# Kernel optimization log

Measured on AMD Instinct MI355X. Metric: run time of the kernel, lower is better.

Reference implementation:

```python
import jax, jax.numpy as jnp
import numpy as np

# Paged/ragged causal prefill attention (FlashInfer wrapper.run semantics),
# modeled as equal-length batched causal GQA attention.
B, S = 2, 2048          # batch, seq_len (T = B*S tokens, flattened)
H, HKV, D = 32, 8, 128  # query heads, kv heads, head dim
G = H // HKV            # GQA group size
SCALE = 0.08838834764831845  # 1/sqrt(D)


def setup_inputs() -> dict:
    key = jax.random.key(0)
    kq, kk, kv = jax.random.split(key, 3)
    q = jax.random.normal(kq, (B * S, H * D), dtype=jnp.float32)
    k = jax.random.normal(kk, (B * S, HKV * D), dtype=jnp.float32)
    v = jax.random.normal(kv, (B * S, HKV * D), dtype=jnp.float32)
    return {"q": q, "k": k, "v": v}


def reference(q, k, v):
    # q: [T, H*D] -> [B, S, HKV, G, D]; k, v: [T, HKV*D] -> [B, S, HKV, D]
    qh = q.reshape(B, S, HKV, G, D)
    kh = k.reshape(B, S, HKV, D)
    vh = v.reshape(B, S, HKV, D)
    # GQA attention scores: [B, HKV, G, Sq, Sk]
    scores = jnp.einsum('bqhgd,bkhd->bhgqk', qh, kh) * SCALE
    causal = jnp.tril(jnp.ones((S, S), dtype=bool))  # query attends to keys <= its position
    scores = jnp.where(causal, scores, jnp.finfo(scores.dtype).min)
    probs = jax.nn.softmax(scores, axis=-1)
    out = jnp.einsum('bhgqk,bkhd->bqhgd', probs, vh)
    # back to flattened token layout [T, H*D]
    return out.reshape(B * S, H * D)
```

## Files before the change

### kernel.cpp

```cpp
#include <hip/hip_runtime.h>


#define B_   2
#define S_   2048
#define H_   32
#define HKV_ 8
#define D_   128
#define SCALEF 0.08838834764831845f
#define COEF  (SCALEF * 1.44269504088896340736f)
#define DEFER_THR 8.0f

typedef float          f32x4 __attribute__((ext_vector_type(4)));
typedef __bf16         bf16x2 __attribute__((ext_vector_type(2)));
typedef __bf16         bf16x8 __attribute__((ext_vector_type(8)));
typedef unsigned short u16x8 __attribute__((ext_vector_type(8)));

#define MFMA16(a, b, c) __builtin_amdgcn_mfma_f32_16x16x32_bf16((a), (b), (c), 0, 0, 0)

#if defined(__has_builtin)
#if __has_builtin(__builtin_amdgcn_exp2f)
#define EXP2F(x) __builtin_amdgcn_exp2f(x)
#endif
#endif
#ifndef EXP2F
#define EXP2F(x) exp2f(x)
#endif

static __device__ __forceinline__ unsigned short f2bf(float f) {
  unsigned int u = __builtin_bit_cast(unsigned int, f);
  u = (u + 0x7fffu + ((u >> 16) & 1u)) >> 16;
  return (unsigned short)u;
}

static __device__ __forceinline__ void load_lds16(const void* g, void* l) {
  __builtin_amdgcn_global_load_lds(
      (const __attribute__((address_space(1))) void*)g,
      (__attribute__((address_space(3))) void*)l, 16, 0, 0);
}

template <int CTRL>
static __device__ __forceinline__ float dppf(float v) {
  return __builtin_bit_cast(
      float, __builtin_amdgcn_update_dpp(0, __builtin_bit_cast(int, v), CTRL,
                                         0xF, 0xF, true));
}
static __device__ __forceinline__ float rowmax16(float v) {
  v = fmaxf(v, dppf<0x128>(v));
  v = fmaxf(v, dppf<0x124>(v));
  v = fmaxf(v, dppf<0x122>(v));
  v = fmaxf(v, dppf<0x121>(v));
  return v;
}
static __device__ __forceinline__ float rowsum16(float v) {
  v += dppf<0x128>(v);
  v += dppf<0x124>(v);
  v += dppf<0x122>(v);
  v += dppf<0x121>(v);
  return v;
}

__global__ __launch_bounds__(256) void k_convert_kernel(
    const float* __restrict__ k, unsigned short* __restrict__ kbf) {
  int t = blockIdx.x * 256 + threadIdx.x;
  int o = t * 8;
  int d = o & (D_ - 1);
  int s = (o >> 7) & (S_ - 1);
  int bh = o >> 18;
  int b = bh >> 3, hkv = bh & 7;
  const float* src = k + (size_t)(b * S_ + s) * (HKV_ * D_) + hkv * D_ + d;
  f32x4 x0 = *(const f32x4*)src;
  f32x4 x1 = *(const f32x4*)(src + 4);
  u16x8 w;
  w[0] = f2bf(x0[0]); w[1] = f2bf(x0[1]); w[2] = f2bf(x0[2]); w[3] = f2bf(x0[3]);
  w[4] = f2bf(x1[0]); w[5] = f2bf(x1[1]); w[6] = f2bf(x1[2]); w[7] = f2bf(x1[3]);
  *(u16x8*)(kbf + o) = w;
}

__global__ __launch_bounds__(256) void vt_transpose_kernel(
    const float* __restrict__ v, unsigned short* __restrict__ vt) {
  __shared__ float tile[32][65];
  const int tid = threadIdx.x;
  const int s0 = blockIdx.x * 64;
  const int d0 = blockIdx.y * 32;
  const int bh = blockIdx.z;
  const float* src = v + (size_t)(bh >> 3) * S_ * (HKV_ * D_) + (bh & 7) * D_;
#pragma unroll
  for (int it = 0; it < 8; ++it) {
    int idx = it * 256 + tid;
    int sl = idx >> 5, dl = idx & 31;
    tile[dl][sl] = src[(size_t)(s0 + sl) * (HKV_ * D_) + d0 + dl];
  }
  __syncthreads();
  unsigned int* dst = (unsigned int*)vt;
#pragma unroll
  for (int it = 0; it < 4; ++it) {
    int idx = it * 256 + tid;
    int dl = idx >> 5, sp = idx & 31;
    unsigned int w = (unsigned int)f2bf(tile[dl][2 * sp]) |
                     ((unsigned int)f2bf(tile[dl][2 * sp + 1]) << 16);
    dst[(((size_t)bh * D_ + d0 + dl) * S_ + s0 + 2 * sp) >> 1] = w;
  }
}

#define PSTR 40

__global__ __launch_bounds__(256, 4) void attn_kernel(
    const float* __restrict__ qg, const unsigned short* __restrict__ kbfg,
    const unsigned short* __restrict__ vtg, float* __restrict__ outg) {
  __shared__ unsigned short KL[2][32 * 128];
  __shared__ unsigned short VL[2][128 * 32];
  __shared__ unsigned short PL[4][16 * PSTR];

  const int tid = threadIdx.x;
  const int wave = tid >> 6, lane = tid & 63;
  const int l15 = lane & 15, quad = lane >> 4;

  const int xb = (int)blockIdx.x;
  const int b = (int)(blockIdx.y >> 5), h = (int)(blockIdx.y & 31);
  const int hkv = h >> 2;

  const unsigned short* kbf = kbfg + (size_t)(b * HKV_ + hkv) * S_ * D_;
  const unsigned short* vtb = vtg + (size_t)(b * HKV_ + hkv) * D_ * S_;

  const f32x4 zero4 = {0.f, 0.f, 0.f, 0.f};
  const float NEG_INF = -__builtin_huge_valf();

  auto stage = [&](int kt, int buf) {
#pragma unroll
    for (int j = 0; j < 2; ++j) {
      int si = wave * 128 + j * 64 + lane;
      int kr = si >> 4, pc = si & 15;
      int lc = pc ^ (kr & 15);
      load_lds16(kbf + (size_t)(kt * 32 + kr) * D_ + lc * 8,
                 &KL[buf][(wave * 128 + j * 64) * 8]);
    }
#pragma unroll
    for (int j = 0; j < 2; ++j) {
      int si = wave * 128 + j * 64 + lane;
      int dr = si >> 2, pc = si & 3;
      int lc = pc ^ ((dr >> 1) & 3);
      load_lds16(vtb + (size_t)dr * S_ + kt * 32 + lc * 8,
                 &VL[buf][(wave * 128 + j * 64) * 8]);
    }
  };

  for (int ph = 0; ph < 2; ++ph) {
    const int qb = ph ? (31 - xb) : xb;
    const int qbase = qb * 64 + wave * 16;

    bf16x8 qf[4];
#pragma unroll
    for (int ch = 0; ch < 4; ++ch) {
      const float* p = qg + (size_t)(b * S_ + qbase + l15) * (H_ * D_) +
                       h * D_ + ch * 32 + quad * 8;
      f32x4 x0 = *(const f32x4*)p;
      f32x4 x1 = *(const f32x4*)(p + 4);
      bf16x8 t;
      t[0] = (__bf16)(x0[0] * COEF); t[1] = (__bf16)(x0[1] * COEF);
      t[2] = (__bf16)(x0[2] * COEF); t[3] = (__bf16)(x0[3] * COEF);
      t[4] = (__bf16)(x1[0] * COEF); t[5] = (__bf16)(x1[1] * COEF);
      t[6] = (__bf16)(x1[2] * COEF); t[7] = (__bf16)(x1[3] * COEF);
      qf[ch] = t;
    }

    f32x4 acc[8];
#pragma unroll
    for (int dt = 0; dt < 8; ++dt) acc[dt] = zero4;
    f32x4 mrow = {NEG_INF, NEG_INF, NEG_INF, NEG_INF};
    f32x4 lsum = zero4;

    const int nkt = qb * 2 + 2;

    stage(0, 0);
    __syncthreads();

    for (int kt = 0; kt < nkt; ++kt) {
      const int cur = kt & 1;
      if (kt + 1 < nkt) stage(kt + 1, cur ^ 1);

      if (kt * 32 <= qbase + 15) {
        f32x4 sc[2] = {zero4, zero4};
#pragma unroll
        for (int h2 = 0; h2 < 2; ++h2) {
          const int row = h2 * 16 + l15;
#pragma unroll
          for (int ch = 0; ch < 4; ++ch) {
            const int pc = (ch * 4 + quad) ^ l15;
            u16x8 kf = *(const u16x8*)&KL[cur][row * D_ + pc * 8];
            sc[h2] = MFMA16(qf[ch], __builtin_bit_cast(bf16x8, kf), sc[h2]);
          }
        }
        const int kb0 = kt * 32;
#pragma unroll
        for (int h2 = 0; h2 < 2; ++h2) {
          if (kb0 + h2 * 16 + 15 > qbase) {
            int kgp = kb0 + h2 * 16 + l15;
#pragma unroll
            for (int r = 0; r < 4; ++r) {
              int qgp = qbase + quad * 4 + r;
              if (kgp > qgp) sc[h2][r] = NEG_INF;
            }
          }
        }
        {
          float a0 = fmaxf(sc[0][0], sc[1][0]) - mrow[0];
          float a1 = fmaxf(sc[0][1], sc[1][1]) - mrow[1];
          float a2 = fmaxf(sc[0][2], sc[1][2]) - mrow[2];
          float a3 = fmaxf(sc[0][3], sc[1][3]) - mrow[3];
          float dmax = fmaxf(fmaxf(a0, a1), fmaxf(a2, a3));
          if (!__all(dmax <= DEFER_THR)) {
            f32x4 al;
#pragma unroll
            for (int r = 0; r < 4; ++r) {
              float mt = rowmax16(fmaxf(sc[0][r], sc[1][r]));
              float mn = fmaxf(mrow[r], mt);
              al[r] = EXP2F(mrow[r] - mn);
              mrow[r] = mn;
              lsum[r] *= al[r];
            }
#pragma unroll
            for (int dt = 0; dt < 8; ++dt)
#pragma unroll
              for (int r = 0; r < 4; ++r) acc[dt][r] *= al[r];
          }
        }
#pragma unroll
        for (int r = 0; r < 4; ++r) {
          float p0 = EXP2F(sc[0][r] - mrow[r]);
          float p1 = EXP2F(sc[1][r] - mrow[r]);
          sc[0][r] = p0;
          sc[1][r] = p1;
          lsum[r] += p0 + p1;
        }
#pragma unroll
        for (int h2 = 0; h2 < 2; ++h2)
#pragma unroll
          for (int r = 0; r < 4; ++r) {
            float mine = sc[h2][r];
            float nb = dppf<0xB1>(mine);
            if (!(l15 & 1)) {
              bf16x2 pk;
              pk[0] = (__bf16)mine;
              pk[1] = (__bf16)nb;
              *(bf16x2*)&PL[wave][(quad * 4 + r) * PSTR + h2 * 16 + l15] = pk;
            }
          }
        u16x8 pf = *(const u16x8*)&PL[wave][l15 * PSTR + quad * 8];
        bf16x8 pb = __builtin_bit_cast(bf16x8, pf);
        const int vsw = (quad ^ ((l15 >> 1) & 3)) * 8;
#pragma unroll
        for (int dt = 0; dt < 8; ++dt) {
          u16x8 vf = *(const u16x8*)&VL[cur][(dt * 16 + l15) * 32 + vsw];
          acc[dt] = MFMA16(pb, __builtin_bit_cast(bf16x8, vf), acc[dt]);
        }
      }
      __syncthreads();
    }

    f32x4 inv;
#pragma unroll
    for (int r = 0; r < 4; ++r) inv[r] = 1.0f / rowsum16(lsum[r]);
#pragma unroll
    for (int dt = 0; dt < 8; ++dt)
#pragma unroll
      for (int r = 0; r < 4; ++r)
        outg[(size_t)(b * S_ + qbase + quad * 4 + r) * (H_ * D_) +
             h * D_ + dt * 16 + l15] = acc[dt][r] * inv[r];
  }
}

extern "C" void kernel_launch(void* const* d_in, const int* in_sizes, int n_in,
                              void* d_out, int out_size, void* d_ws,
                              size_t ws_size, hipStream_t stream) {
  const float* q = (const float*)d_in[0];
  const float* k = (const float*)d_in[1];
  const float* v = (const float*)d_in[2];
  float* out = (float*)d_out;
  unsigned short* kws = (unsigned short*)d_ws;
  unsigned short* vtws = kws + (size_t)B_ * HKV_ * S_ * D_;

  k_convert_kernel<<<(B_ * S_ * HKV_ * D_ / 8) / 256, 256, 0, stream>>>(k, kws);

  dim3 g1(S_ / 64, D_ / 32, B_ * HKV_);
  vt_transpose_kernel<<<g1, 256, 0, stream>>>(v, vtws);

  dim3 g2(16, B_ * H_);
  attn_kernel<<<g2, 256, 0, stream>>>(q, kws, vtws, out);
}
```

Before: 241.0 us.

## Use 64-key tiles, transposed score MFMA, and XCD-aware block mapping

Doubles the key/value tile per iteration to 64 keys, which halves the number of barriers and staging rounds. It computes scores as K·Q so that each lane owns a single query row. Per-row max and sum then reduce with ds_swizzle/bpermute instead of four DPP steps per row, and P is written to LDS as packed 4-element stores. Block IDs are remapped so that blocks sharing a KV head land on the same XCD for L2 reuse. In exchange it doubles LDS use and lowers the occupancy hint to 2 blocks per CU.

```diff
diff --git a/kernel.cpp b/kernel.cpp
--- a/kernel.cpp
+++ b/kernel.cpp
@@ -11,7 +11,7 @@
 #define DEFER_THR 8.0f
 
 typedef float          f32x4 __attribute__((ext_vector_type(4)));
-typedef __bf16         bf16x2 __attribute__((ext_vector_type(2)));
+typedef __bf16         bf16x4 __attribute__((ext_vector_type(4)));
 typedef __bf16         bf16x8 __attribute__((ext_vector_type(8)));
 typedef unsigned short u16x8 __attribute__((ext_vector_type(8)));
 
@@ -38,25 +38,14 @@
       (__attribute__((address_space(3))) void*)l, 16, 0, 0);
 }
 
-template <int CTRL>
-static __device__ __forceinline__ float dppf(float v) {
+static __device__ __forceinline__ float swz_x16(float v) {
   return __builtin_bit_cast(
-      float, __builtin_amdgcn_update_dpp(0, __builtin_bit_cast(int, v), CTRL,
-                                         0xF, 0xF, true));
-}
-static __device__ __forceinline__ float rowmax16(float v) {
-  v = fmaxf(v, dppf<0x128>(v));
-  v = fmaxf(v, dppf<0x124>(v));
-  v = fmaxf(v, dppf<0x122>(v));
-  v = fmaxf(v, dppf<0x121>(v));
-  return v;
-}
-static __device__ __forceinline__ float rowsum16(float v) {
-  v += dppf<0x128>(v);
-  v += dppf<0x124>(v);
-  v += dppf<0x122>(v);
-  v += dppf<0x121>(v);
-  return v;
+      float, __builtin_amdgcn_ds_swizzle(__builtin_bit_cast(int, v), 0x401F));
+}
+static __device__ __forceinline__ float bperm_f(int byteaddr, float v) {
+  return __builtin_bit_cast(
+      float,
+      __builtin_amdgcn_ds_bpermute(byteaddr, __builtin_bit_cast(int, v)));
 }
 
 __global__ __launch_bounds__(256) void k_convert_kernel(
@@ -102,22 +91,29 @@
   }
 }
 
-#define PSTR 40
-
-__global__ __launch_bounds__(256, 4) void attn_kernel(
+#define PSTR 72
+
+__global__ __launch_bounds__(256, 2) void attn_kernel(
     const float* __restrict__ qg, const unsigned short* __restrict__ kbfg,
     const unsigned short* __restrict__ vtg, float* __restrict__ outg) {
-  __shared__ unsigned short KL[2][32 * 128];
-  __shared__ unsigned short VL[2][128 * 32];
+  __shared__ unsigned short KL[2][2][32 * 128];
+  __shared__ unsigned short VL[2][2][128 * 32];
   __shared__ unsigned short PL[4][16 * PSTR];
 
   const int tid = threadIdx.x;
   const int wave = tid >> 6, lane = tid & 63;
   const int l15 = lane & 15, quad = lane >> 4;
-
-  const int xb = (int)blockIdx.x;
-  const int b = (int)(blockIdx.y >> 5), h = (int)(blockIdx.y & 31);
-  const int hkv = h >> 2;
+  const int a32 = ((lane ^ 32) << 2);
+  const int rowa = quad << 4;
+
+  const int id = (int)blockIdx.x + 16 * (int)blockIdx.y;
+  const int xcd = id & 7, slot = id >> 3;
+  const int bhkv = xcd * 2 + (slot >> 6);
+  const int inner = slot & 63;
+  const int g = inner >> 4;
+  const int xb = inner & 15;
+  const int b = bhkv >> 3, hkv = bhkv & 7;
+  const int h = hkv * 4 + g;
 
   const unsigned short* kbf = kbfg + (size_t)(b * HKV_ + hkv) * S_ * D_;
   const unsigned short* vtb = vtg + (size_t)(b * HKV_ + hkv) * D_ * S_;
@@ -127,26 +123,31 @@
 
   auto stage = [&](int kt, int buf) {
 #pragma unroll
-    for (int j = 0; j < 2; ++j) {
-      int si = wave * 128 + j * 64 + lane;
-      int kr = si >> 4, pc = si & 15;
-      int lc = pc ^ (kr & 15);
-      load_lds16(kbf + (size_t)(kt * 32 + kr) * D_ + lc * 8,
-                 &KL[buf][(wave * 128 + j * 64) * 8]);
-    }
-#pragma unroll
-    for (int j = 0; j < 2; ++j) {
-      int si = wave * 128 + j * 64 + lane;
-      int dr = si >> 2, pc = si & 3;
-      int lc = pc ^ ((dr >> 1) & 3);
-      load_lds16(vtb + (size_t)dr * S_ + kt * 32 + lc * 8,
-                 &VL[buf][(wave * 128 + j * 64) * 8]);
-    }
+    for (int sub = 0; sub < 2; ++sub)
+#pragma unroll
+      for (int j = 0; j < 2; ++j) {
+        int si = wave * 128 + j * 64 + lane;
+        int kr = si >> 4, pc = si & 15;
+        int lc = pc ^ (kr & 15);
+        load_lds16(kbf + (size_t)(kt * 64 + sub * 32 + kr) * D_ + lc * 8,
+                   &KL[buf][sub][(wave * 128 + j * 64) * 8]);
+      }
+#pragma unroll
+    for (int sub = 0; sub < 2; ++sub)
+#pragma unroll
+      for (int j = 0; j < 2; ++j) {
+        int si = wave * 128 + j * 64 + lane;
+        int dr = si >> 2, pc = si & 3;
+        int lc = pc ^ ((dr >> 1) & 3);
+        load_lds16(vtb + (size_t)dr * S_ + kt * 64 + sub * 32 + lc * 8,
+                   &VL[buf][sub][(wave * 128 + j * 64) * 8]);
+      }
   };
 
   for (int ph = 0; ph < 2; ++ph) {
     const int qb = ph ? (31 - xb) : xb;
     const int qbase = qb * 64 + wave * 16;
+    const int qgp = qbase + l15;
 
     bf16x8 qf[4];
 #pragma unroll
@@ -166,10 +167,10 @@
     f32x4 acc[8];
 #pragma unroll
     for (int dt = 0; dt < 8; ++dt) acc[dt] = zero4;
-    f32x4 mrow = {NEG_INF, NEG_INF, NEG_INF, NEG_INF};
-    f32x4 lsum = zero4;
-
-    const int nkt = qb * 2 + 2;
+    float mrow = NEG_INF;
+    float lsum = 0.f;
+
+    const int nkt = qb + 1;
 
     stage(0, 0);
     __syncthreads();
@@ -178,88 +179,87 @@
       const int cur = kt & 1;
       if (kt + 1 < nkt) stage(kt + 1, cur ^ 1);
 
-      if (kt * 32 <= qbase + 15) {
-        f32x4 sc[2] = {zero4, zero4};
-#pragma unroll
-        for (int h2 = 0; h2 < 2; ++h2) {
-          const int row = h2 * 16 + l15;
+      if (kt * 64 <= qbase + 15) {
+        f32x4 sc[4] = {zero4, zero4, zero4, zero4};
+#pragma unroll
+        for (int h2 = 0; h2 < 4; ++h2) {
+          const unsigned short* KS =
+              &KL[cur][h2 >> 1][((h2 & 1) * 16 + l15) * D_];
 #pragma unroll
           for (int ch = 0; ch < 4; ++ch) {
             const int pc = (ch * 4 + quad) ^ l15;
-            u16x8 kf = *(const u16x8*)&KL[cur][row * D_ + pc * 8];
-            sc[h2] = MFMA16(qf[ch], __builtin_bit_cast(bf16x8, kf), sc[h2]);
+            u16x8 kf = *(const u16x8*)&KS[pc * 8];
+            sc[h2] = MFMA16(__builtin_bit_cast(bf16x8, kf), qf[ch], sc[h2]);
           }
         }
-        const int kb0 = kt * 32;
-#pragma unroll
-        for (int h2 = 0; h2 < 2; ++h2) {
+        const int kb0 = kt * 64;
+#pragma unroll
+        for (int h2 = 0; h2 < 4; ++h2) {
           if (kb0 + h2 * 16 + 15 > qbase) {
-            int kgp = kb0 + h2 * 16 + l15;
+            int kb2 = kb0 + h2 * 16 + quad * 4;
 #pragma unroll
             for (int r = 0; r < 4; ++r) {
-              int qgp = qbase + quad * 4 + r;
-              if (kgp > qgp) sc[h2][r] = NEG_INF;
+              if (kb2 + r > qgp) sc[h2][r] = NEG_INF;
             }
           }
         }
-        {
-          float a0 = fmaxf(sc[0][0], sc[1][0]) - mrow[0];
-          float a1 = fmaxf(sc[0][1], sc[1][1]) - mrow[1];
-          float a2 = fmaxf(sc[0][2], sc[1][2]) - mrow[2];
-          float a3 = fmaxf(sc[0][3], sc[1][3]) - mrow[3];
-          float dmax = fmaxf(fmaxf(a0, a1), fmaxf(a2, a3));
-          if (!__all(dmax <= DEFER_THR)) {
-            f32x4 al;
-#pragma unroll
-            for (int r = 0; r < 4; ++r) {
-              float mt = rowmax16(fmaxf(sc[0][r], sc[1][r]));
-              float mn = fmaxf(mrow[r], mt);
-              al[r] = EXP2F(mrow[r] - mn);
-              mrow[r] = mn;
-              lsum[r] *= al[r];
-            }
-#pragma unroll
-            for (int dt = 0; dt < 8; ++dt)
-#pragma unroll
-              for (int r = 0; r < 4; ++r) acc[dt][r] *= al[r];
+        float l8 = NEG_INF;
+#pragma unroll
+        for (int h2 = 0; h2 < 4; ++h2)
+          l8 = fmaxf(l8, fmaxf(fmaxf(sc[h2][0], sc[h2][1]),
+                               fmaxf(sc[h2][2], sc[h2][3])));
+        if (!__all(l8 <= mrow + DEFER_THR)) {
+          float t = fmaxf(l8, swz_x16(l8));
+          t = fmaxf(t, bperm_f(a32, t));
+          float mn = fmaxf(mrow, t);
+          float al = EXP2F(mrow - mn);
+          mrow = mn;
+          lsum *= al;
+          f32x4 av;
+#pragma unroll
+          for (int r = 0; r < 4; ++r) av[r] = bperm_f(rowa + (r << 2), al);
+#pragma unroll
+          for (int dt = 0; dt < 8; ++dt)
+#pragma unroll
+            for (int r = 0; r < 4; ++r) acc[dt][r] *= av[r];
+        }
+#pragma unroll
+        for (int h2 = 0; h2 < 4; ++h2)
+#pragma unroll
+          for (int r = 0; r < 4; ++r) sc[h2][r] = EXP2F(sc[h2][r] - mrow);
+#pragma unroll
+        for (int h2 = 0; h2 < 4; ++h2)
+          lsum += (sc[h2][0] + sc[h2][1]) + (sc[h2][2] + sc[h2][3]);
+#pragma unroll
+        for (int h2 = 0; h2 < 4; ++h2) {
+          bf16x4 w;
+          w[0] = (__bf16)sc[h2][0]; w[1] = (__bf16)sc[h2][1];
+          w[2] = (__bf16)sc[h2][2]; w[3] = (__bf16)sc[h2][3];
+          *(bf16x4*)&PL[wave][l15 * PSTR + h2 * 16 + quad * 4] = w;
+        }
+#pragma unroll
+        for (int kh = 0; kh < 2; ++kh) {
+          u16x8 pf = *(const u16x8*)&PL[wave][l15 * PSTR + kh * 32 + quad * 8];
+          bf16x8 pb = __builtin_bit_cast(bf16x8, pf);
+          const int vsw = (quad ^ ((l15 >> 1) & 3)) * 8;
+#pragma unroll
+          for (int dt = 0; dt < 8; ++dt) {
+            u16x8 vf =
+                *(const u16x8*)&VL[cur][kh][(dt * 16 + l15) * 32 + vsw];
+            acc[dt] = MFMA16(pb, __builtin_bit_cast(bf16x8, vf), acc[dt]);
           }
-        }
-#pragma unroll
-        for (int r = 0; r < 4; ++r) {
-          float p0 = EXP2F(sc[0][r] - mrow[r]);
-          float p1 = EXP2F(sc[1][r] - mrow[r]);
-          sc[0][r] = p0;
-          sc[1][r] = p1;
-          lsum[r] += p0 + p1;
-        }
-#pragma unroll
-        for (int h2 = 0; h2 < 2; ++h2)
-#pragma unroll
-          for (int r = 0; r < 4; ++r) {
-            float mine = sc[h2][r];
-            float nb = dppf<0xB1>(mine);
-            if (!(l15 & 1)) {
-              bf16x2 pk;
-              pk[0] = (__bf16)mine;
-              pk[1] = (__bf16)nb;
-              *(bf16x2*)&PL[wave][(quad * 4 + r) * PSTR + h2 * 16 + l15] = pk;
-            }
-          }
-        u16x8 pf = *(const u16x8*)&PL[wave][l15 * PSTR + quad * 8];
-        bf16x8 pb = __builtin_bit_cast(bf16x8, pf);
-        const int vsw = (quad ^ ((l15 >> 1) & 3)) * 8;
-#pragma unroll
-        for (int dt = 0; dt < 8; ++dt) {
-          u16x8 vf = *(const u16x8*)&VL[cur][(dt * 16 + l15) * 32 + vsw];
-          acc[dt] = MFMA16(pb, __builtin_bit_cast(bf16x8, vf), acc[dt]);
         }
       }
       __syncthreads();
     }
 
+    float s = lsum;
+    s += swz_x16(s);
+    s += bperm_f(a32, s);
+    float linv = 1.0f / s;
     f32x4 inv;
 #pragma unroll
-    for (int r = 0; r < 4; ++r) inv[r] = 1.0f / rowsum16(lsum[r]);
+    for (int r = 0; r < 4; ++r) inv[r] = bperm_f(rowa + (r << 2), linv);
 #pragma unroll
     for (int dt = 0; dt < 8; ++dt)
 #pragma unroll
```

Measured after the change: 240.3 us. Within noise of the previous version (-0.3%).
